# Performance work log

Measured on AMD Instinct MI355X. Metric: run time of the kernel, lower is better.

The kernel has to match this reference:

```python
import jax, jax.numpy as jnp
import numpy as np

B, S, ENC_UNITS, DEC_UNITS, NUM_UNITS = 64, 2048, 512, 512, 512


def setup_inputs() -> dict:
    key = jax.random.key(0)
    k_h, k_eo, k_w1, k_b1, k_w2, k_b2, k_v, k_bv = jax.random.split(key, 8)
    sd = 0.05
    return {
        "H": jax.random.normal(k_h, (B, DEC_UNITS), dtype=jnp.float32),
        "EO": jax.random.normal(k_eo, (B, S, ENC_UNITS), dtype=jnp.float32),
        "W1": jax.random.normal(k_w1, (ENC_UNITS, NUM_UNITS), dtype=jnp.float32) * sd,
        "b1": jnp.zeros((NUM_UNITS,), dtype=jnp.float32),
        "W2": jax.random.normal(k_w2, (DEC_UNITS, NUM_UNITS), dtype=jnp.float32) * sd,
        "b2": jnp.zeros((NUM_UNITS,), dtype=jnp.float32),
        "V": jax.random.normal(k_v, (NUM_UNITS, 1), dtype=jnp.float32) * sd,
        "bv": jnp.zeros((1,), dtype=jnp.float32),
    }


def reference(H, EO, W1, b1, W2, b2, V, bv):
    # H: [B, D], EO: [B, S, E]
    # score = V(tanh(W1(EO) + W2(H)[:, None, :]))  -> [B, S, 1]
    w1_eo = jnp.einsum("bse,eu->bsu", EO, W1) + b1          # [B, S, U]
    w2_h = (H @ W2 + b2)[:, None, :]                          # [B, 1, U]
    score = jnp.tanh(w1_eo + w2_h) @ V + bv                   # [B, S, 1]
    attention_weights = jax.nn.softmax(score, axis=1)         # [B, S, 1]
    context_vector = jnp.sum(attention_weights * EO, axis=1)  # [B, E]
    return context_vector, attention_weights
```

## Files before the change

### kernel.cpp

```cpp
#include <hip/hip_runtime.h>
#include <hip/hip_bf16.h>


typedef __attribute__((ext_vector_type(8))) short bf16x8;
typedef __attribute__((ext_vector_type(4))) short bf16x4;
typedef __attribute__((ext_vector_type(4))) float f32x4;

#define NB 64
#define NS 2048
#define NE 512
#define NU 512

__device__ __forceinline__ unsigned short f2bf(float f) {
  union { float f; unsigned int u; } x; x.f = f;
  unsigned int u = x.u;
  unsigned int r = (u + 0x7fffu + ((u >> 16) & 1u)) >> 16;
  return (unsigned short)r;
}

__device__ __forceinline__ float tanh_fast(float x) {
  x = fminf(fmaxf(x, -15.f), 15.f);
  float e = __expf(2.f * x);
  return 1.f - 2.f / (e + 1.f);
}

__global__ __launch_bounds__(256) void pack_w1_kernel(
    const float* __restrict__ W1, unsigned short* __restrict__ W1p) {
  int t = blockIdx.x * 256 + threadIdx.x;
  int k = t >> 9, n = t & 511;
  int kt = k >> 5, kr = k & 31;
  int quad = kr >> 3, j = kr & 7;
  int l = (quad << 4) | (n & 15);
  int nt = n >> 4;
  int dst = ((((nt << 4) + kt) * 64 + l) << 3) + j;
  W1p[dst] = f2bf(W1[t]);
}

__global__ __launch_bounds__(512) void compute_c_kernel(
    const float* __restrict__ H, const float* __restrict__ W2,
    const float* __restrict__ b1, const float* __restrict__ b2,
    float* __restrict__ cvec) {
  const int b = blockIdx.x, u = threadIdx.x;
  __shared__ float hs[512];
  hs[u] = H[(b << 9) + u];
  __syncthreads();
  float s = 0.f;
#pragma unroll 8
  for (int d = 0; d < 512; d++) s = fmaf(hs[d], W2[(d << 9) + u], s);
  cvec[(b << 9) + u] = s + b1[u] + b2[u];
}

__global__ __launch_bounds__(256, 2) void scores_kernel(
    const float* __restrict__ EO, const unsigned short* __restrict__ W1p,
    const float* __restrict__ cvec, const float* __restrict__ V,
    const float* __restrict__ bv, float* __restrict__ scores) {
  __shared__ unsigned short As[128 * 264];
  __shared__ float cs[512];
  __shared__ float vs[512];

  const int tid = threadIdx.x;
  const int bx = blockIdx.x;
  const int b = bx >> 4;
  const int s0 = (bx & 15) << 7;

  cs[tid] = cvec[(b << 9) + tid];
  cs[tid + 256] = cvec[(b << 9) + 256 + tid];
  vs[tid] = V[tid];
  vs[tid + 256] = V[256 + tid];

  const int lane = tid & 63, wave = tid >> 6;
  const int quad = lane >> 4, col = lane & 15;

  const float* eo_base = EO + ((size_t)(b * NS + s0)) * NE;

  bf16x8 afrag[2][16];

  for (int ph = 0; ph < 2; ph++) {
    if (ph) __syncthreads();
#pragma unroll
    for (int it = 0; it < 32; it++) {
      int idx = (it * 256 + tid) * 4;
      int row = idx >> 8;
      int c = idx & 255;
      const float4* src =
          reinterpret_cast<const float4*>(eo_base + (size_t)row * NE + ph * 256 + c);
      float4 f = *src;
      bf16x4 h;
      h.x = (short)f2bf(f.x); h.y = (short)f2bf(f.y);
      h.z = (short)f2bf(f.z); h.w = (short)f2bf(f.w);
      *reinterpret_cast<bf16x4*>(&As[row * 264 + c]) = h;
    }
    __syncthreads();
#pragma unroll
    for (int kk = 0; kk < 8; kk++) {
      int koff = kk * 32 + quad * 8;
      afrag[0][ph * 8 + kk] =
          *reinterpret_cast<const bf16x8*>(&As[(wave * 32 + col) * 264 + koff]);
      afrag[1][ph * 8 + kk] =
          *reinterpret_cast<const bf16x8*>(&As[(wave * 32 + 16 + col) * 264 + koff]);
    }
  }

  float sacc[2][4] = {{0.f, 0.f, 0.f, 0.f}, {0.f, 0.f, 0.f, 0.f}};
  const bf16x8* Wp = reinterpret_cast<const bf16x8*>(W1p);
  const float bvv = bv[0];

  for (int nt = 0; nt < 32; nt++) {
    f32x4 acc0 = {0.f, 0.f, 0.f, 0.f};
    f32x4 acc1 = {0.f, 0.f, 0.f, 0.f};
    const bf16x8* p = Wp + nt * 1024 + lane;
#pragma unroll
    for (int kt = 0; kt < 16; kt++) {
      bf16x8 bfr = p[kt * 64];
      acc0 = __builtin_amdgcn_mfma_f32_16x16x32_bf16(afrag[0][kt], bfr, acc0, 0, 0, 0);
      acc1 = __builtin_amdgcn_mfma_f32_16x16x32_bf16(afrag[1][kt], bfr, acc1, 0, 0, 0);
    }
    int u = (nt << 4) + col;
    float cu = cs[u], vu = vs[u];
#pragma unroll
    for (int r = 0; r < 4; r++) {
      sacc[0][r] += tanh_fast(acc0[r] + cu) * vu;
      sacc[1][r] += tanh_fast(acc1[r] + cu) * vu;
    }
  }

#pragma unroll
  for (int m = 1; m < 16; m <<= 1) {
#pragma unroll
    for (int t = 0; t < 2; t++)
#pragma unroll
      for (int r = 0; r < 4; r++)
        sacc[t][r] += __shfl_xor(sacc[t][r], m, 64);
  }
  if (col == 0) {
#pragma unroll
    for (int t = 0; t < 2; t++)
#pragma unroll
      for (int r = 0; r < 4; r++)
        scores[(size_t)b * NS + s0 + wave * 32 + t * 16 + quad * 4 + r] =
            sacc[t][r] + bvv;
  }
}

__global__ __launch_bounds__(256) void softmax_kernel(float* __restrict__ w) {
  const int b = blockIdx.x, tid = threadIdx.x;
  float* row = w + (size_t)b * NS;
  float v[8];
  float mx = -1e30f;
#pragma unroll
  for (int i = 0; i < 8; i++) { v[i] = row[i * 256 + tid]; mx = fmaxf(mx, v[i]); }
#pragma unroll
  for (int off = 32; off; off >>= 1) mx = fmaxf(mx, __shfl_xor(mx, off, 64));
  __shared__ float redm[4], reds[4];
  const int wv = tid >> 6, ln = tid & 63;
  if (ln == 0) redm[wv] = mx;
  __syncthreads();
  mx = fmaxf(fmaxf(redm[0], redm[1]), fmaxf(redm[2], redm[3]));
  float s = 0.f;
#pragma unroll
  for (int i = 0; i < 8; i++) { v[i] = __expf(v[i] - mx); s += v[i]; }
#pragma unroll
  for (int off = 32; off; off >>= 1) s += __shfl_xor(s, off, 64);
  if (ln == 0) reds[wv] = s;
  __syncthreads();
  s = reds[0] + reds[1] + reds[2] + reds[3];
  float inv = 1.f / s;
#pragma unroll
  for (int i = 0; i < 8; i++) row[i * 256 + tid] = v[i] * inv;
}

__global__ __launch_bounds__(256) void context_kernel(
    const float* __restrict__ EO, const float* __restrict__ w,
    float* __restrict__ ctx) {
  const int b = blockIdx.x, sc = blockIdx.y, tid = threadIdx.x;
  __shared__ float wl[256];
  wl[tid] = w[(size_t)b * NS + sc * 256 + tid];
  __syncthreads();
  const float2* eo2 =
      reinterpret_cast<const float2*>(EO + ((size_t)b * NS + sc * 256) * NE) + tid;
  float ax = 0.f, ay = 0.f;
#pragma unroll 8
  for (int i = 0; i < 256; i++) {
    float2 e = eo2[(size_t)i * 256];
    float wt = wl[i];
    ax = fmaf(wt, e.x, ax);
    ay = fmaf(wt, e.y, ay);
  }
  atomicAdd(&ctx[(b << 9) + tid * 2], ax);
  atomicAdd(&ctx[(b << 9) + tid * 2 + 1], ay);
}

extern "C" void kernel_launch(void* const* d_in, const int* in_sizes, int n_in,
                              void* d_out, int out_size, void* d_ws, size_t ws_size,
                              hipStream_t stream) {
  (void)in_sizes; (void)n_in; (void)out_size; (void)ws_size;
  const float* H  = (const float*)d_in[0];
  const float* EO = (const float*)d_in[1];
  const float* W1 = (const float*)d_in[2];
  const float* b1 = (const float*)d_in[3];
  const float* W2 = (const float*)d_in[4];
  const float* b2 = (const float*)d_in[5];
  const float* V  = (const float*)d_in[6];
  const float* bv = (const float*)d_in[7];

  float* out_ctx = (float*)d_out;
  float* out_w   = (float*)d_out + NB * NE;

  unsigned short* W1p = (unsigned short*)d_ws;
  float* cvec = (float*)((char*)d_ws + 512 * 1024);

  hipMemsetAsync(out_ctx, 0, (size_t)NB * NE * sizeof(float), stream);
  pack_w1_kernel<<<1024, 256, 0, stream>>>(W1, W1p);
  compute_c_kernel<<<NB, 512, 0, stream>>>(H, W2, b1, b2, cvec);
  scores_kernel<<<1024, 256, 0, stream>>>(EO, W1p, cvec, V, bv, out_w);
  softmax_kernel<<<NB, 256, 0, stream>>>(out_w);
  context_kernel<<<dim3(NB, 8), 256, 0, stream>>>(EO, out_w, out_ctx);
}
```

Measured before the change: 607.9 us.

## Fuse context reduction into scores kernel with flash-style partial softmax

Merges the score, softmax and context computations. Each strip block computes a local max, its exponent sum and a weighted EO partial sum from the bf16 fragments it already holds in registers, and a small combine kernel rescales and merges the partials. This removes the second full read of EO and two kernel launches. W1 tiles are also staged through double-buffered LDS, and EO is loaded straight into MFMA fragments without going through shared memory. The context is now accumulated from bf16-rounded EO, which lowers its precision.

Result: slower. 825.1 us (+35.7%).

```diff
diff --git a/kernel.cpp b/kernel.cpp
--- a/kernel.cpp
+++ b/kernel.cpp
@@ -3,7 +3,6 @@
 
 
 typedef __attribute__((ext_vector_type(8))) short bf16x8;
-typedef __attribute__((ext_vector_type(4))) short bf16x4;
 typedef __attribute__((ext_vector_type(4))) float f32x4;
 
 #define NB 64
@@ -16,6 +15,12 @@
   unsigned int u = x.u;
   unsigned int r = (u + 0x7fffu + ((u >> 16) & 1u)) >> 16;
   return (unsigned short)r;
+}
+
+__device__ __forceinline__ float bf2f(short s) {
+  union { unsigned int u; float f; } x;
+  x.u = ((unsigned int)(unsigned short)s) << 16;
+  return x.f;
 }
 
 __device__ __forceinline__ float tanh_fast(float x) {
@@ -50,144 +55,206 @@
   cvec[(b << 9) + u] = s + b1[u] + b2[u];
 }
 
-__global__ __launch_bounds__(256, 2) void scores_kernel(
+__global__ __launch_bounds__(256, 2) void scores_ctx_kernel(
     const float* __restrict__ EO, const unsigned short* __restrict__ W1p,
     const float* __restrict__ cvec, const float* __restrict__ V,
-    const float* __restrict__ bv, float* __restrict__ scores) {
-  __shared__ unsigned short As[128 * 264];
-  __shared__ float cs[512];
-  __shared__ float vs[512];
+    float* __restrict__ scores, float* __restrict__ m_ws,
+    float* __restrict__ l_ws, float* __restrict__ ck_ws) {
+  __shared__ __align__(16) unsigned short Bs[2][16384];
+  __shared__ float cs[512], vs[512];
+  __shared__ float sc_l[128], p_l[128];
+  __shared__ __align__(16) float cpartw[4][512];
+  __shared__ float m_sh, lw[2];
 
   const int tid = threadIdx.x;
-  const int bx = blockIdx.x;
-  const int b = bx >> 4;
-  const int s0 = (bx & 15) << 7;
+  const int b = blockIdx.x >> 4;
+  const int strip = blockIdx.x & 15;
+  const int s0 = strip << 7;
+  const int lane = tid & 63, wave = tid >> 6;
+  const int quad = lane >> 4, col = lane & 15;
 
   cs[tid] = cvec[(b << 9) + tid];
   cs[tid + 256] = cvec[(b << 9) + 256 + tid];
   vs[tid] = V[tid];
   vs[tid + 256] = V[256 + tid];
 
-  const int lane = tid & 63, wave = tid >> 6;
-  const int quad = lane >> 4, col = lane & 15;
-
-  const float* eo_base = EO + ((size_t)(b * NS + s0)) * NE;
-
   bf16x8 afrag[2][16];
-
-  for (int ph = 0; ph < 2; ph++) {
-    if (ph) __syncthreads();
-#pragma unroll
-    for (int it = 0; it < 32; it++) {
-      int idx = (it * 256 + tid) * 4;
-      int row = idx >> 8;
-      int c = idx & 255;
-      const float4* src =
-          reinterpret_cast<const float4*>(eo_base + (size_t)row * NE + ph * 256 + c);
-      float4 f = *src;
-      bf16x4 h;
-      h.x = (short)f2bf(f.x); h.y = (short)f2bf(f.y);
-      h.z = (short)f2bf(f.z); h.w = (short)f2bf(f.w);
-      *reinterpret_cast<bf16x4*>(&As[row * 264 + c]) = h;
+  {
+    const float* r0 =
+        EO + ((size_t)(b * NS + s0 + wave * 32 + col)) * NE + quad * 8;
+    const float* r1 = r0 + 16 * NE;
+#pragma unroll
+    for (int kt = 0; kt < 16; kt++) {
+      float4 x0 = *(const float4*)(r0 + kt * 32);
+      float4 y0 = *(const float4*)(r0 + kt * 32 + 4);
+      float4 x1 = *(const float4*)(r1 + kt * 32);
+      float4 y1 = *(const float4*)(r1 + kt * 32 + 4);
+      union { short s[8]; bf16x8 v; } u0, u1;
+      u0.s[0] = (short)f2bf(x0.x); u0.s[1] = (short)f2bf(x0.y);
+      u0.s[2] = (short)f2bf(x0.z); u0.s[3] = (short)f2bf(x0.w);
+      u0.s[4] = (short)f2bf(y0.x); u0.s[5] = (short)f2bf(y0.y);
+      u0.s[6] = (short)f2bf(y0.z); u0.s[7] = (short)f2bf(y0.w);
+      u1.s[0] = (short)f2bf(x1.x); u1.s[1] = (short)f2bf(x1.y);
+      u1.s[2] = (short)f2bf(x1.z); u1.s[3] = (short)f2bf(x1.w);
+      u1.s[4] = (short)f2bf(y1.x); u1.s[5] = (short)f2bf(y1.y);
+      u1.s[6] = (short)f2bf(y1.z); u1.s[7] = (short)f2bf(y1.w);
+      afrag[0][kt] = u0.v;
+      afrag[1][kt] = u1.v;
+    }
+  }
+
+  const uint4* W1p4 = (const uint4*)W1p;
+#pragma unroll
+  for (int i = 0; i < 8; i++)
+    ((uint4*)&Bs[0][0])[i * 256 + tid] = W1p4[i * 256 + tid];
+  __syncthreads();
+
+  float sacc[2][4] = {{0.f, 0.f, 0.f, 0.f}, {0.f, 0.f, 0.f, 0.f}};
+
+  for (int it = 0; it < 16; it++) {
+    const int cur = it & 1;
+    uint4 breg[8];
+    if (it < 15) {
+#pragma unroll
+      for (int i = 0; i < 8; i++)
+        breg[i] = W1p4[(it + 1) * 2048 + i * 256 + tid];
+    }
+#pragma unroll
+    for (int half = 0; half < 2; half++) {
+      const int nt = it * 2 + half;
+      f32x4 acc0 = {0.f, 0.f, 0.f, 0.f};
+      f32x4 acc1 = {0.f, 0.f, 0.f, 0.f};
+      const bf16x8* bp = (const bf16x8*)&Bs[cur][half * 8192];
+#pragma unroll
+      for (int kt = 0; kt < 16; kt++) {
+        bf16x8 bfr = bp[kt * 64 + lane];
+        acc0 = __builtin_amdgcn_mfma_f32_16x16x32_bf16(afrag[0][kt], bfr, acc0, 0, 0, 0);
+        acc1 = __builtin_amdgcn_mfma_f32_16x16x32_bf16(afrag[1][kt], bfr, acc1, 0, 0, 0);
+      }
+      int u = (nt << 4) + col;
+      float cu = cs[u], vu = vs[u];
+#pragma unroll
+      for (int r = 0; r < 4; r++) {
+        sacc[0][r] += tanh_fast(acc0[r] + cu) * vu;
+        sacc[1][r] += tanh_fast(acc1[r] + cu) * vu;
+      }
+    }
+    if (it < 15) {
+#pragma unroll
+      for (int i = 0; i < 8; i++)
+        ((uint4*)&Bs[cur ^ 1][0])[i * 256 + tid] = breg[i];
     }
     __syncthreads();
-#pragma unroll
-    for (int kk = 0; kk < 8; kk++) {
-      int koff = kk * 32 + quad * 8;
-      afrag[0][ph * 8 + kk] =
-          *reinterpret_cast<const bf16x8*>(&As[(wave * 32 + col) * 264 + koff]);
-      afrag[1][ph * 8 + kk] =
-          *reinterpret_cast<const bf16x8*>(&As[(wave * 32 + 16 + col) * 264 + koff]);
-    }
-  }
-
-  float sacc[2][4] = {{0.f, 0.f, 0.f, 0.f}, {0.f, 0.f, 0.f, 0.f}};
-  const bf16x8* Wp = reinterpret_cast<const bf16x8*>(W1p);
-  const float bvv = bv[0];
-
-  for (int nt = 0; nt < 32; nt++) {
-    f32x4 acc0 = {0.f, 0.f, 0.f, 0.f};
-    f32x4 acc1 = {0.f, 0.f, 0.f, 0.f};
-    const bf16x8* p = Wp + nt * 1024 + lane;
-#pragma unroll
-    for (int kt = 0; kt < 16; kt++) {
-      bf16x8 bfr = p[kt * 64];
-      acc0 = __builtin_amdgcn_mfma_f32_16x16x32_bf16(afrag[0][kt], bfr, acc0, 0, 0, 0);
-      acc1 = __builtin_amdgcn_mfma_f32_16x16x32_bf16(afrag[1][kt], bfr, acc1, 0, 0, 0);
-    }
-    int u = (nt << 4) + col;
-    float cu = cs[u], vu = vs[u];
-#pragma unroll
-    for (int r = 0; r < 4; r++) {
-      sacc[0][r] += tanh_fast(acc0[r] + cu) * vu;
-      sacc[1][r] += tanh_fast(acc1[r] + cu) * vu;
-    }
-  }
-
-#pragma unroll
-  for (int m = 1; m < 16; m <<= 1) {
+  }
+
+#pragma unroll
+  for (int m = 1; m < 16; m <<= 1)
 #pragma unroll
     for (int t = 0; t < 2; t++)
 #pragma unroll
       for (int r = 0; r < 4; r++)
         sacc[t][r] += __shfl_xor(sacc[t][r], m, 64);
-  }
+
   if (col == 0) {
 #pragma unroll
     for (int t = 0; t < 2; t++)
 #pragma unroll
-      for (int r = 0; r < 4; r++)
-        scores[(size_t)b * NS + s0 + wave * 32 + t * 16 + quad * 4 + r] =
-            sacc[t][r] + bvv;
-  }
-}
-
-__global__ __launch_bounds__(256) void softmax_kernel(float* __restrict__ w) {
+      for (int r = 0; r < 4; r++) {
+        int row = wave * 32 + t * 16 + quad * 4 + r;
+        sc_l[row] = sacc[t][r];
+        scores[(size_t)b * NS + s0 + row] = sacc[t][r];
+      }
+  }
+  __syncthreads();
+
+  if (wave == 0) {
+    float m0 = fmaxf(sc_l[lane], sc_l[lane + 64]);
+#pragma unroll
+    for (int off = 32; off; off >>= 1) m0 = fmaxf(m0, __shfl_xor(m0, off, 64));
+    if (lane == 0) m_sh = m0;
+  }
+  __syncthreads();
+  const float mstrip = m_sh;
+
+  if (tid < 128) {
+    float p = __expf(sc_l[tid] - mstrip);
+    p_l[tid] = p;
+#pragma unroll
+    for (int off = 32; off; off >>= 1) p += __shfl_xor(p, off, 64);
+    if (lane == 0) lw[wave] = p;
+  }
+  __syncthreads();
+  if (tid == 0) {
+    m_ws[b * 16 + strip] = mstrip;
+    l_ws[b * 16 + strip] = lw[0] + lw[1];
+  }
+
+  const float p0 = p_l[wave * 32 + col];
+  const float p1 = p_l[wave * 32 + 16 + col];
+#pragma unroll
+  for (int kt = 0; kt < 16; kt++) {
+    float v[8];
+#pragma unroll
+    for (int j = 0; j < 8; j++)
+      v[j] = p0 * bf2f(afrag[0][kt][j]) + p1 * bf2f(afrag[1][kt][j]);
+#pragma unroll
+    for (int m = 1; m < 16; m <<= 1)
+#pragma unroll
+      for (int j = 0; j < 8; j++) v[j] += __shfl_xor(v[j], m, 64);
+    if (col == 0) {
+      float* dst = &cpartw[wave][kt * 32 + quad * 8];
+      *(float4*)dst = make_float4(v[0], v[1], v[2], v[3]);
+      *(float4*)(dst + 4) = make_float4(v[4], v[5], v[6], v[7]);
+    }
+  }
+  __syncthreads();
+
+  {
+    float2 s = {0.f, 0.f};
+#pragma unroll
+    for (int w = 0; w < 4; w++) {
+      float2 t = *(const float2*)&cpartw[w][tid * 2];
+      s.x += t.x; s.y += t.y;
+    }
+    *(float2*)&ck_ws[((size_t)(b * 16 + strip)) * 512 + tid * 2] = s;
+  }
+}
+
+__global__ __launch_bounds__(256) void combine_kernel(
+    const float* __restrict__ m_ws, const float* __restrict__ l_ws,
+    const float* __restrict__ ck_ws, float* __restrict__ ctx,
+    float* __restrict__ w ) {
   const int b = blockIdx.x, tid = threadIdx.x;
+  __shared__ float msh[16], lsh[16];
+  if (tid < 16) {
+    msh[tid] = m_ws[b * 16 + tid];
+    lsh[tid] = l_ws[b * 16 + tid];
+  }
+  __syncthreads();
+  float M = msh[0];
+#pragma unroll
+  for (int k = 1; k < 16; k++) M = fmaxf(M, msh[k]);
+  float L = 0.f;
+#pragma unroll
+  for (int k = 0; k < 16; k++) L += lsh[k] * __expf(msh[k] - M);
+  const float invL = 1.f / L;
+
+  float2 acc = {0.f, 0.f};
+#pragma unroll
+  for (int k = 0; k < 16; k++) {
+    float sc = __expf(msh[k] - M);
+    float2 t = *(const float2*)&ck_ws[((size_t)(b * 16 + k)) * 512 + tid * 2];
+    acc.x += sc * t.x; acc.y += sc * t.y;
+  }
+  acc.x *= invL; acc.y *= invL;
+  *(float2*)&ctx[(b << 9) + tid * 2] = acc;
+
   float* row = w + (size_t)b * NS;
-  float v[8];
-  float mx = -1e30f;
-#pragma unroll
-  for (int i = 0; i < 8; i++) { v[i] = row[i * 256 + tid]; mx = fmaxf(mx, v[i]); }
-#pragma unroll
-  for (int off = 32; off; off >>= 1) mx = fmaxf(mx, __shfl_xor(mx, off, 64));
-  __shared__ float redm[4], reds[4];
-  const int wv = tid >> 6, ln = tid & 63;
-  if (ln == 0) redm[wv] = mx;
-  __syncthreads();
-  mx = fmaxf(fmaxf(redm[0], redm[1]), fmaxf(redm[2], redm[3]));
-  float s = 0.f;
-#pragma unroll
-  for (int i = 0; i < 8; i++) { v[i] = __expf(v[i] - mx); s += v[i]; }
-#pragma unroll
-  for (int off = 32; off; off >>= 1) s += __shfl_xor(s, off, 64);
-  if (ln == 0) reds[wv] = s;
-  __syncthreads();
-  s = reds[0] + reds[1] + reds[2] + reds[3];
-  float inv = 1.f / s;
-#pragma unroll
-  for (int i = 0; i < 8; i++) row[i * 256 + tid] = v[i] * inv;
-}
-
-__global__ __launch_bounds__(256) void context_kernel(
-    const float* __restrict__ EO, const float* __restrict__ w,
-    float* __restrict__ ctx) {
-  const int b = blockIdx.x, sc = blockIdx.y, tid = threadIdx.x;
-  __shared__ float wl[256];
-  wl[tid] = w[(size_t)b * NS + sc * 256 + tid];
-  __syncthreads();
-  const float2* eo2 =
-      reinterpret_cast<const float2*>(EO + ((size_t)b * NS + sc * 256) * NE) + tid;
-  float ax = 0.f, ay = 0.f;
-#pragma unroll 8
-  for (int i = 0; i < 256; i++) {
-    float2 e = eo2[(size_t)i * 256];
-    float wt = wl[i];
-    ax = fmaf(wt, e.x, ax);
-    ay = fmaf(wt, e.y, ay);
-  }
-  atomicAdd(&ctx[(b << 9) + tid * 2], ax);
-  atomicAdd(&ctx[(b << 9) + tid * 2 + 1], ay);
+#pragma unroll
+  for (int i = 0; i < 8; i++) {
+    float s = row[i * 256 + tid];
+    row[i * 256 + tid] = __expf(s - M) * invL;
+  }
 }
 
 extern "C" void kernel_launch(void* const* d_in, const int* in_sizes, int n_in,
@@ -201,18 +268,20 @@
   const float* W2 = (const float*)d_in[4];
   const float* b2 = (const float*)d_in[5];
   const float* V  = (const float*)d_in[6];
-  const float* bv = (const float*)d_in[7];
 
   float* out_ctx = (float*)d_out;
   float* out_w   = (float*)d_out + NB * NE;
 
-  unsigned short* W1p = (unsigned short*)d_ws;
-  float* cvec = (float*)((char*)d_ws + 512 * 1024);
-
-  hipMemsetAsync(out_ctx, 0, (size_t)NB * NE * sizeof(float), stream);
+  char* ws = (char*)d_ws;
+  unsigned short* W1p = (unsigned short*)ws;
+  float* cvec = (float*)(ws + 512 * 1024);
+  float* m_ws = (float*)(ws + 640 * 1024);
+  float* l_ws = (float*)(ws + 644 * 1024);
+  float* ck_ws = (float*)(ws + 656 * 1024);
+
   pack_w1_kernel<<<1024, 256, 0, stream>>>(W1, W1p);
   compute_c_kernel<<<NB, 512, 0, stream>>>(H, W2, b1, b2, cvec);
-  scores_kernel<<<1024, 256, 0, stream>>>(EO, W1p, cvec, V, bv, out_w);
-  softmax_kernel<<<NB, 256, 0, stream>>>(out_w);
-  context_kernel<<<dim3(NB, 8), 256, 0, stream>>>(EO, out_w, out_ctx);
-}
+  scores_ctx_kernel<<<1024, 256, 0, stream>>>(EO, W1p, cvec, V, out_w,
+                                              m_ws, l_ws, ck_ws);
+  combine_kernel<<<NB, 256, 0, stream>>>(m_ws, l_ws, ck_ws, out_ctx, out_w);
+}
```
